# Kernel optimization log

Measured on AMD Instinct MI355X. Metric: run time of the kernel, lower is better.

## Reference

```python
import math
import jax, jax.numpy as jnp
import numpy as np

B, N, G, D = 8, 1000, 1000, 2
E, H = 128, 8           # embedding_dim, n_heads
DH = E // H             # head dim
KNN = 16                # n_decoding_neighbors (static: mask all zeros -> K=min(16,N))
TANH_CLIP = 10.0


def make_heads(x, n_heads):
    # (B, n, E) -> (B, n_heads, n, E//n_heads)
    b, n, e = x.shape
    return x.reshape(b, n, n_heads, e // n_heads).transpose(0, 2, 1, 3)


def setup_inputs() -> dict:
    key = jax.random.key(0)
    ks = jax.random.split(key, 12)
    s = 1.0 / math.sqrt(E)
    return {
        "last_node": jax.random.randint(ks[0], (B, G), 0, N),
        "coordinates": jax.random.uniform(ks[1], (B, N, D), dtype=jnp.float32),
        "embeddings": jax.random.normal(ks[2], (B, N, E), dtype=jnp.float32),
        "group_ninf_mask": jnp.zeros((B, G, N), dtype=jnp.float32),
        "Wq_graph": jax.random.normal(ks[3], (E, E), dtype=jnp.float32) * s,
        "Wq_first": jax.random.normal(ks[4], (E, E), dtype=jnp.float32) * s,
        "Wq_last": jax.random.normal(ks[5], (E, E), dtype=jnp.float32) * s,
        "Wk": jax.random.normal(ks[6], (E, E), dtype=jnp.float32) * s,
        "Wv": jax.random.normal(ks[7], (E, E), dtype=jnp.float32) * s,
        "W_comb": jax.random.normal(ks[8], (E, E), dtype=jnp.float32) * s,
        "b_comb": jax.random.normal(ks[9], (E,), dtype=jnp.float32) * s,
    }


def reference(last_node, coordinates, embeddings, group_ninf_mask,
              Wq_graph, Wq_first, Wq_last, Wk, Wv, W_comb, b_comb):
    # --- reset() precomputation ---
    graph_emb = embeddings.mean(axis=1, keepdims=True)          # (B,1,E)
    q_graph = make_heads(graph_emb @ Wq_graph.T, H)             # (B,H,1,DH)
    k_h = make_heads(embeddings @ Wk.T, H)                      # (B,H,N,DH)
    v_h = make_heads(embeddings @ Wv.T, H)                      # (B,H,N,DH)

    # --- gather last node embedding ---
    idx_e = jnp.broadcast_to(last_node[..., None], (B, G, E))
    last_emb = jnp.take_along_axis(embeddings, idx_e, axis=1)   # (B,G,E)
    q_first = make_heads(last_emb @ Wq_first.T, H)              # (B,H,G,DH)
    q_last = make_heads(last_emb @ Wq_last.T, H)
    glimpse_q = q_graph + q_first + q_last                      # (B,H,G,DH)

    # --- KNN neighbor mask (cdist + topk + scatter) ---
    idx_c = jnp.broadcast_to(last_node[..., None], (B, G, D))
    last_coord = jnp.take_along_axis(coordinates, idx_c, axis=1)  # (B,G,D)
    d2 = (jnp.sum(last_coord**2, -1)[:, :, None]
          + jnp.sum(coordinates**2, -1)[:, None, :]
          - 2.0 * jnp.einsum('bgd,bnd->bgn', last_coord, coordinates))
    dist = jnp.sqrt(jnp.maximum(d2, 0.0))                       # (B,G,N)
    dist = jnp.where(group_ninf_mask == -jnp.inf, jnp.inf, dist)
    _, knn_idx = jax.lax.top_k(-dist, KNN)                      # (B,G,K) smallest dists
    bi = jnp.arange(B)[:, None, None]
    gi = jnp.arange(G)[None, :, None]
    glimpse_mask = jnp.full((B, G, N), -jnp.inf, dtype=jnp.float32)
    glimpse_mask = glimpse_mask.at[bi, gi, knn_idx].set(0.0)

    # --- masked multi-head glimpse attention ---
    scores = jnp.einsum('bhgd,bhnd->bhgn', glimpse_q, k_h) / math.sqrt(DH)
    scores = scores + glimpse_mask[:, None, :, :]
    attn = jax.nn.softmax(scores, axis=-1)
    out = jnp.einsum('bhgn,bhnd->bhgd', attn, v_h)              # (B,H,G,DH)
    out = out.transpose(0, 2, 1, 3).reshape(B, G, E)
    final_q = out @ W_comb.T + b_comb                           # (B,G,E)

    # --- tanh-clipped scoring + softmax ---
    score = jnp.einsum('bge,bne->bgn', final_q, embeddings) / math.sqrt(E)
    score_masked = TANH_CLIP * jnp.tanh(score) + group_ninf_mask
    probs = jax.nn.softmax(score_masked, axis=2)                # (B,G,N)
    return probs
```

## Files before the change

kernel.cpp:

```cpp
#include <hip/hip_runtime.h>
#include <math.h>

#define BD 8
#define NN 1000
#define GG 1000
#define EE 128

typedef unsigned long long u64;
typedef __attribute__((ext_vector_type(8))) short short8;
typedef __attribute__((ext_vector_type(4))) float f32x4;

#define OFF_QG    0
#define OFF_K     1024
#define OFF_V     (OFF_K + 1024000)
#define OFF_QFL   (OFF_V + 1024000)
#define OFF_OUTG  (OFF_QFL + 1024000)
#define OFF_FQ    (OFF_OUTG + 1024000)
#define OFF_PART  (OFF_FQ + 1024000)
#define OFF_GPART (OFF_PART + 64000)

__global__ __launch_bounds__(256) void k_gq1(const float* __restrict__ emb,
                                             float* __restrict__ gpart) {
  __shared__ float ps[2][128];
  int b = blockIdx.x, blk = blockIdx.y;
  int t = threadIdx.x;
  int e = t & 127, p = t >> 7;
  const float* eb = emb + ((size_t)b * NN + blk * 40 + p * 20) * EE + e;
  float s = 0.f;
#pragma unroll 4
  for (int n = 0; n < 20; ++n) s += eb[(size_t)n * EE];
  ps[p][e] = s;
  __syncthreads();
  if (t < 128) gpart[(b * 25 + blk) * 128 + t] = ps[0][t] + ps[1][t];
}

__global__ __launch_bounds__(128) void k_gq2(const float* __restrict__ gpart,
                                             const float* __restrict__ Wqg,
                                             float* __restrict__ qg) {
  __shared__ float ge[128];
  int b = blockIdx.x, t = threadIdx.x;
  float s = 0.f;
#pragma unroll 5
  for (int j = 0; j < 25; ++j) s += gpart[(b * 25 + j) * 128 + t];
  ge[t] = s * (1.f / 1000.f);
  __syncthreads();
  const float* wr = Wqg + (size_t)t * EE;
  float acc = 0.f;
#pragma unroll 8
  for (int k = 0; k < 128; ++k) acc += ge[k] * wr[k];
  qg[b * EE + t] = acc;
}

__global__ __launch_bounds__(256) void k_proj(const float* __restrict__ emb,
                                              const float* __restrict__ Wk,
                                              const float* __restrict__ Wv,
                                              const float* __restrict__ Wqf,
                                              const float* __restrict__ Wql,
                                              float* __restrict__ Karr,
                                              float* __restrict__ Varr,
                                              float* __restrict__ QFL) {
  __shared__ float Als[16][68];
  __shared__ float Bls[16][68];
  int mt = blockIdx.x, nt = blockIdx.y;
  int t = threadIdx.x;
  int ty = t >> 4, tx = t & 15;
  int row4 = t >> 2, kq = t & 3;
  float acc[4][4] = {};
  for (int k0 = 0; k0 < 128; k0 += 16) {
    const float* ap = emb + (size_t)(mt * 64 + row4) * EE + k0 + kq * 4;
    float4 av = *(const float4*)ap;
    int j = nt * 64 + row4;
    float4 bv;
    if (j < 128) {
      bv = *(const float4*)(Wk + (size_t)j * EE + k0 + kq * 4);
    } else if (j < 256) {
      bv = *(const float4*)(Wv + (size_t)(j - 128) * EE + k0 + kq * 4);
    } else {
      float4 f = *(const float4*)(Wqf + (size_t)(j - 256) * EE + k0 + kq * 4);
      float4 l = *(const float4*)(Wql + (size_t)(j - 256) * EE + k0 + kq * 4);
      bv = make_float4(f.x + l.x, f.y + l.y, f.z + l.z, f.w + l.w);
    }
    Als[kq * 4 + 0][row4] = av.x; Als[kq * 4 + 1][row4] = av.y;
    Als[kq * 4 + 2][row4] = av.z; Als[kq * 4 + 3][row4] = av.w;
    Bls[kq * 4 + 0][row4] = bv.x; Bls[kq * 4 + 1][row4] = bv.y;
    Bls[kq * 4 + 2][row4] = bv.z; Bls[kq * 4 + 3][row4] = bv.w;
    __syncthreads();
#pragma unroll
    for (int k = 0; k < 16; ++k) {
      float a0 = Als[k][ty * 4 + 0], a1 = Als[k][ty * 4 + 1];
      float a2 = Als[k][ty * 4 + 2], a3 = Als[k][ty * 4 + 3];
      float b0 = Bls[k][tx * 4 + 0], b1 = Bls[k][tx * 4 + 1];
      float b2 = Bls[k][tx * 4 + 2], b3 = Bls[k][tx * 4 + 3];
      acc[0][0] += a0 * b0; acc[0][1] += a0 * b1; acc[0][2] += a0 * b2; acc[0][3] += a0 * b3;
      acc[1][0] += a1 * b0; acc[1][1] += a1 * b1; acc[1][2] += a1 * b2; acc[1][3] += a1 * b3;
      acc[2][0] += a2 * b0; acc[2][1] += a2 * b1; acc[2][2] += a2 * b2; acc[2][3] += a2 * b3;
      acc[3][0] += a3 * b0; acc[3][1] += a3 * b1; acc[3][2] += a3 * b2; acc[3][3] += a3 * b3;
    }
    __syncthreads();
  }
  float* outp; int cb;
  if (nt < 2)      { outp = Karr; cb = nt * 64; }
  else if (nt < 4) { outp = Varr; cb = (nt - 2) * 64; }
  else             { outp = QFL;  cb = (nt - 4) * 64; }
#pragma unroll
  for (int i = 0; i < 4; ++i) {
    int r = mt * 64 + ty * 4 + i;
    float4 v = make_float4(acc[i][0], acc[i][1], acc[i][2], acc[i][3]);
    *(float4*)(outp + (size_t)r * EE + cb + tx * 4) = v;
  }
}

template <int CTRL>
__device__ __forceinline__ unsigned dpp_minu(unsigned x) {
  unsigned o = (unsigned)__builtin_amdgcn_update_dpp(0, (int)x, CTRL, 0xf, 0xf, false);
  return o < x ? o : x;
}
__device__ __forceinline__ unsigned wave_min_u32(unsigned x) {
  x = dpp_minu<0x121>(x);
  x = dpp_minu<0x122>(x);
  x = dpp_minu<0x124>(x);
  x = dpp_minu<0x128>(x);
  unsigned o = (unsigned)__shfl_xor((int)x, 16); x = o < x ? o : x;
  o = (unsigned)__shfl_xor((int)x, 32); x = o < x ? o : x;
  return x;
}

__global__ __launch_bounds__(256) void k_glimpse(const int* __restrict__ last_node,
                                                 const float* __restrict__ coords,
                                                 const float* __restrict__ mask,
                                                 const float* __restrict__ qg,
                                                 const float* __restrict__ QFL,
                                                 const float* __restrict__ Karr,
                                                 const float* __restrict__ Varr,
                                                 float* __restrict__ outg) {
  __shared__ float pbuf[4][128];
  __shared__ int   nbuf[4][16];
  const float INF = __builtin_inff();
  int wv = threadIdx.x >> 6;
  int lane = threadIdx.x & 63;
  int wid = (blockIdx.x * blockDim.x + threadIdx.x) >> 6;
  int b = wid / GG, g = wid % GG;
  int last = last_node[b * GG + g];
  const float2* cb2 = (const float2*)(coords + (size_t)b * NN * 2);
  float2 lc = cb2[last];
  float lc2 = lc.x * lc.x + lc.y * lc.y;
  const float* mrow = mask + ((size_t)b * GG + g) * NN;
  unsigned d2u[16];
#pragma unroll
  for (int i = 0; i < 16; ++i) {
    int n = lane + (i << 6);
    unsigned k = 0xFFFFFFFFu;
    if (n < NN) {
      float2 c = cb2[n];
      float d2 = lc2 + (c.x * c.x + c.y * c.y) - 2.f * (lc.x * c.x + lc.y * c.y);
      d2 = fmaxf(d2, 0.f);
      k = __float_as_uint(d2);
      if (mrow[n] == -INF) k = 0x7F800000u;
    }
    d2u[i] = k;
  }
  int h = lane >> 3;
  int kk = lane & 7;
  int n0sel = 0, n1sel = 0;
  for (int s = 0; s < 16; ++s) {
    unsigned bv = d2u[0]; int bs = 0;
#pragma unroll
    for (int i = 1; i < 16; ++i) {
      bool better = d2u[i] < bv;
      bv = better ? d2u[i] : bv;
      bs = better ? i : bs;
    }
    unsigned wm = wave_min_u32(bv);
    u64 tied = __ballot(bv == wm);
    int wn;
    if (__popcll(tied) == 1) {
      int wl = (int)__builtin_ctzll(tied);
      int ws = __builtin_amdgcn_readlane(bs, wl);
      wn = wl + (ws << 6);
    } else {
      unsigned cn = (bv == wm) ? (unsigned)(lane + (bs << 6)) : 0x7FFFFFFFu;
      cn = wave_min_u32(cn);
      wn = (int)__builtin_amdgcn_readfirstlane((int)cn);
    }
    n0sel = (s == kk) ? wn : n0sel;
    n1sel = (s == kk + 8) ? wn : n1sel;
    int iw = wn >> 6;
    bool me = (lane == (wn & 63));
#pragma unroll
    for (int i = 0; i < 16; ++i)
      if (i == iw && me) d2u[i] = 0xFFFFFFFFu;
  }
  float qh[16];
  {
    const float4* qg4 = (const float4*)(qg + b * EE + h * 16);
    const float4* qf4 = (const float4*)(QFL + ((size_t)b * NN + last) * EE + h * 16);
#pragma unroll
    for (int u = 0; u < 4; ++u) {
      float4 a = qg4[u], c = qf4[u];
      qh[u * 4 + 0] = a.x + c.x; qh[u * 4 + 1] = a.y + c.y;
      qh[u * 4 + 2] = a.z + c.z; qh[u * 4 + 3] = a.w + c.w;
    }
  }
  const float* Kb = Karr + (size_t)b * NN * EE;
  float s0 = 0.f, s1 = 0.f;
  {
    const float4* k04 = (const float4*)(Kb + (size_t)n0sel * EE + h * 16);
    const float4* k14 = (const float4*)(Kb + (size_t)n1sel * EE + h * 16);
    float4 ka[4], kb[4];
#pragma unroll
    for (int u = 0; u < 4; ++u) { ka[u] = k04[u]; kb[u] = k14[u]; }
#pragma unroll
    for (int u = 0; u < 4; ++u) {
      s0 += qh[u * 4 + 0] * ka[u].x; s0 += qh[u * 4 + 1] * ka[u].y;
      s0 += qh[u * 4 + 2] * ka[u].z; s0 += qh[u * 4 + 3] * ka[u].w;
      s1 += qh[u * 4 + 0] * kb[u].x; s1 += qh[u * 4 + 1] * kb[u].y;
      s1 += qh[u * 4 + 2] * kb[u].z; s1 += qh[u * 4 + 3] * kb[u].w;
    }
  }
  s0 *= 0.25f; s1 *= 0.25f;
  float m = fmaxf(s0, s1);
#pragma unroll
  for (int off = 1; off < 8; off <<= 1) m = fmaxf(m, __shfl_xor(m, off));
  float e0 = __expf(s0 - m), e1 = __expf(s1 - m);
  float se = e0 + e1;
#pragma unroll
  for (int off = 1; off < 8; off <<= 1) se += __shfl_xor(se, off);
  float p0 = e0 / se, p1 = e1 / se;
  pbuf[wv][h * 16 + kk] = p0;
  pbuf[wv][h * 16 + kk + 8] = p1;
  if (h == 0) { nbuf[wv][kk] = n0sel; nbuf[wv][kk + 8] = n1sel; }
  const float* Vb = Varr + (size_t)b * NN * EE;
  float o0 = 0.f, o1 = 0.f;
#pragma unroll
  for (int c = 0; c < 2; ++c) {
    int nk[8]; float pk[8]; float2 vv[8];
#pragma unroll
    for (int j = 0; j < 8; ++j) { nk[j] = nbuf[wv][c * 8 + j]; pk[j] = pbuf[wv][h * 16 + c * 8 + j]; }
#pragma unroll
    for (int j = 0; j < 8; ++j)
      vv[j] = *(const float2*)(Vb + (size_t)nk[j] * EE + h * 16 + kk * 2);
#pragma unroll
    for (int j = 0; j < 8; ++j) { o0 += pk[j] * vv[j].x; o1 += pk[j] * vv[j].y; }
  }
  *(float2*)(outg + ((size_t)b * GG + g) * EE + h * 16 + kk * 2) = make_float2(o0, o1);
}

__global__ __launch_bounds__(256) void k_comb(const float* __restrict__ outg,
                                              const float* __restrict__ Wc,
                                              const float* __restrict__ bc,
                                              short* __restrict__ fq3) {
  __shared__ float Als[16][68];
  __shared__ float Bls[16][132];
  int mt = blockIdx.x;
  int t = threadIdx.x;
  int ty = t >> 4, tx = t & 15;
  int la = t >> 2, akq = t & 3;
  int lb = t >> 1, bkq = t & 1;
  const float* apos = outg + (size_t)(mt * 64 + la) * EE + akq * 4;
  const float* bpos = Wc + (size_t)lb * EE + bkq * 8;
  float acc[4][8] = {};
  float4 pa  = *(const float4*)apos;
  float4 pb0 = *(const float4*)bpos;
  float4 pb1 = *(const float4*)(bpos + 4);
  for (int k0 = 0; k0 < 128; k0 += 16) {
    __syncthreads();
    Als[akq * 4 + 0][la] = pa.x;  Als[akq * 4 + 1][la] = pa.y;
    Als[akq * 4 + 2][la] = pa.z;  Als[akq * 4 + 3][la] = pa.w;
    Bls[bkq * 8 + 0][lb] = pb0.x; Bls[bkq * 8 + 1][lb] = pb0.y;
    Bls[bkq * 8 + 2][lb] = pb0.z; Bls[bkq * 8 + 3][lb] = pb0.w;
    Bls[bkq * 8 + 4][lb] = pb1.x; Bls[bkq * 8 + 5][lb] = pb1.y;
    Bls[bkq * 8 + 6][lb] = pb1.z; Bls[bkq * 8 + 7][lb] = pb1.w;
    __syncthreads();
    if (k0 < 112) {
      pa  = *(const float4*)(apos + k0 + 16);
      pb0 = *(const float4*)(bpos + k0 + 16);
      pb1 = *(const float4*)(bpos + k0 + 20);
    }
#pragma unroll
    for (int k = 0; k < 16; ++k) {
      float4 av  = *(const float4*)&Als[k][ty * 4];
      float4 bv0 = *(const float4*)&Bls[k][tx * 8];
      float4 bv1 = *(const float4*)&Bls[k][tx * 8 + 4];
      float af[4] = {av.x, av.y, av.z, av.w};
      float bf[8] = {bv0.x, bv0.y, bv0.z, bv0.w, bv1.x, bv1.y, bv1.z, bv1.w};
#pragma unroll
      for (int i = 0; i < 4; ++i)
#pragma unroll
        for (int j = 0; j < 8; ++j) acc[i][j] += af[i] * bf[j];
    }
  }
  int c0 = tx * 8;
  float4 b0 = *(const float4*)(bc + c0);
  float4 b1 = *(const float4*)(bc + c0 + 4);
  float bias[8] = {b0.x, b0.y, b0.z, b0.w, b1.x, b1.y, b1.z, b1.w};
  int k0f = tx >> 2;
  int lsub = tx & 3;
#pragma unroll
  for (int i = 0; i < 4; ++i) {
    int r = mt * 64 + ty * 4 + i;
    int b = r / GG;
    int g = r - b * GG;
    short8 hv, mv, lv;
#pragma unroll
    for (int j = 0; j < 8; ++j) {
      float xv = acc[i][j] + bias[j];
      unsigned uh = __float_as_uint(xv) & 0xFFFF0000u;
      hv[j] = (short)(uh >> 16);
      float r1 = xv - __uint_as_float(uh);
      unsigned um = __float_as_uint(r1) & 0xFFFF0000u;
      mv[j] = (short)(um >> 16);
      float r2 = r1 - __uint_as_float(um);
      lv[j] = (short)(__float_as_uint(r2) >> 16);
    }
    int tile = g >> 4;
    int lanefrag = (g & 15) + lsub * 16;
    short* dbase = fq3 + ((size_t)b * 393216 + (size_t)((tile * 4 + k0f) * 3) * 512 + lanefrag * 8);
    *(short8*)(dbase)        = hv;
    *(short8*)(dbase + 512)  = mv;
    *(short8*)(dbase + 1024) = lv;
  }
}

__global__ __launch_bounds__(256) void k_cvt(const float* __restrict__ src,
                                             short* __restrict__ dst) {
  int t = blockIdx.x, b = blockIdx.y;
  int w = threadIdx.x >> 6, l = threadIdx.x & 63;
  int r = min(t * 16 + (l & 15), NN - 1);
  int k = w * 32 + (l >> 4) * 8;
  const float* sp = src + ((size_t)b * NN + r) * EE + k;
  float4 v0 = *(const float4*)sp;
  float4 v1 = *(const float4*)(sp + 4);
  float x[8] = {v0.x, v0.y, v0.z, v0.w, v1.x, v1.y, v1.z, v1.w};
  short8 hv, mv, lv;
#pragma unroll
  for (int j = 0; j < 8; ++j) {
    float xv = x[j];
    unsigned uh = __float_as_uint(xv) & 0xFFFF0000u;
    hv[j] = (short)(uh >> 16);
    float r1 = xv - __uint_as_float(uh);
    unsigned um = __float_as_uint(r1) & 0xFFFF0000u;
    mv[j] = (short)(um >> 16);
    float r2 = r1 - __uint_as_float(um);
    lv[j] = (short)(__float_as_uint(r2) >> 16);
  }
  short* dbase = dst + ((size_t)b * 393216 + (size_t)((t * 4 + w) * 3) * 512 + l * 8);
  *(short8*)(dbase)        = hv;
  *(short8*)(dbase + 512)  = mv;
  *(short8*)(dbase + 1024) = lv;
}

__global__ __launch_bounds__(256, 2) void k_score(const short* __restrict__ fq3,
                                                  const short* __restrict__ emb3,
                                                  const float* __restrict__ mask,
                                                  float* __restrict__ out,
                                                  float* __restrict__ part) {
  __shared__ float xs[4][16][132];
  int nt = blockIdx.x, gt = blockIdx.y, b = blockIdx.z;
  int w = threadIdx.x >> 6, l = threadIdx.x & 63;
  int gtile = gt * 4 + w;
  const short* ab = fq3 + ((size_t)b * 393216 + (size_t)gtile * 6144 + l * 8);
  const short* bb = emb3 + ((size_t)b * 393216 + (size_t)nt * 8 * 6144 + l * 8);
  f32x4 acc[8] = {};
#pragma unroll
  for (int k0 = 0; k0 < 4; ++k0) {
    short8 ah = *(const short8*)(ab + (k0 * 3 + 0) * 512);
    short8 am = *(const short8*)(ab + (k0 * 3 + 1) * 512);
    short8 al = *(const short8*)(ab + (k0 * 3 + 2) * 512);
#pragma unroll
    for (int c = 0; c < 8; ++c) {
      const short* bp = bb + (size_t)(c * 6144 + k0 * 1536);
      short8 bh = *(const short8*)(bp);
      short8 bm = *(const short8*)(bp + 512);
      short8 bl = *(const short8*)(bp + 1024);
      acc[c] = __builtin_amdgcn_mfma_f32_16x16x32_bf16(ah, bh, acc[c], 0, 0, 0);
      acc[c] = __builtin_amdgcn_mfma_f32_16x16x32_bf16(am, bh, acc[c], 0, 0, 0);
      acc[c] = __builtin_amdgcn_mfma_f32_16x16x32_bf16(ah, bm, acc[c], 0, 0, 0);
      acc[c] = __builtin_amdgcn_mfma_f32_16x16x32_bf16(am, bm, acc[c], 0, 0, 0);
      acc[c] = __builtin_amdgcn_mfma_f32_16x16x32_bf16(al, bh, acc[c], 0, 0, 0);
      acc[c] = __builtin_amdgcn_mfma_f32_16x16x32_bf16(ah, bl, acc[c], 0, 0, 0);
    }
  }
  int q = l >> 4, cl = l & 15;
#pragma unroll
  for (int c = 0; c < 8; ++c)
#pragma unroll
    for (int r = 0; r < 4; ++r)
      xs[w][q * 4 + r][c * 16 + cl] = acc[c][r];
  const float rs = 0.08838834764831845f;
  const float NEGINF = -__builtin_inff();
  int half = l >> 5, ln = l & 31;
  int n0 = nt * 128 + ln * 4;
  bool nv = (n0 < NN);
  size_t brow = (size_t)b * GG;
#pragma unroll
  for (int it = 0; it < 8; ++it) {
    int row = it * 2 + half;
    int g = gt * 64 + w * 16 + row;
    bool gv = (g < GG);
    size_t roff = (brow + (gv ? g : GG - 1)) * (size_t)NN;
    f32x4 v = *(const f32x4*)&xs[w][row][ln * 4];
    float4 mvv;
    if (gv && nv) mvv = *(const float4*)(mask + roff + n0);
    else mvv = make_float4(NEGINF, NEGINF, NEGINF, NEGINF);
    float mva[4] = {mvv.x, mvv.y, mvv.z, mvv.w};
    float e[4];
    float rsum = 0.f;
#pragma unroll
    for (int j = 0; j < 4; ++j) {
      float sc = v[j] * rs;
      float u = __expf(2.f * sc);
      float th = 1.f - 2.f * __builtin_amdgcn_rcpf(u + 1.f);
      e[j] = __expf(10.f * th + mva[j]);
      rsum += e[j];
    }
    if (gv && nv) *(float4*)(out + roff + n0) = make_float4(e[0], e[1], e[2], e[3]);
#pragma unroll
    for (int off = 1; off < 32; off <<= 1) rsum += __shfl_xor(rsum, off);
    if (ln == 0 && gv) part[(brow + g) * 8 + nt] = rsum;
  }
}

__global__ __launch_bounds__(256) void k_norm(const float* __restrict__ part,
                                              float* __restrict__ out) {
  int row = blockIdx.x;
  __shared__ float ssum;
  int t = threadIdx.x;
  float v = (t < 8) ? part[(size_t)row * 8 + t] : 0.f;
#pragma unroll
  for (int off = 1; off < 8; off <<= 1) v += __shfl_xor(v, off);
  if (t == 0) ssum = v;
  __syncthreads();
  float inv = 1.f / ssum;
  if (t < 250) {
    float4* o = (float4*)(out + (size_t)row * NN);
    float4 x = o[t];
    x.x *= inv; x.y *= inv; x.z *= inv; x.w *= inv;
    o[t] = x;
  }
}

extern "C" void kernel_launch(void* const* d_in, const int* in_sizes, int n_in,
                              void* d_out, int out_size, void* d_ws, size_t ws_size,
                              hipStream_t stream) {
  const int*   last_node = (const int*)d_in[0];
  const float* coords    = (const float*)d_in[1];
  const float* emb       = (const float*)d_in[2];
  const float* mask      = (const float*)d_in[3];
  const float* Wqg       = (const float*)d_in[4];
  const float* Wqf       = (const float*)d_in[5];
  const float* Wql       = (const float*)d_in[6];
  const float* Wk        = (const float*)d_in[7];
  const float* Wv        = (const float*)d_in[8];
  const float* Wc        = (const float*)d_in[9];
  const float* bc        = (const float*)d_in[10];
  float* out = (float*)d_out;
  float* ws  = (float*)d_ws;

  float* qg    = ws + OFF_QG;
  float* Karr  = ws + OFF_K;
  float* Varr  = ws + OFF_V;
  float* QFL   = ws + OFF_QFL;
  float* outg  = ws + OFF_OUTG;
  float* part  = ws + OFF_PART;
  float* gpart = ws + OFF_GPART;
  short* emb3  = (short*)(ws + OFF_K);
  short* fq3   = (short*)(ws + OFF_FQ);

  k_gq1<<<dim3(BD, 25), dim3(256), 0, stream>>>(emb, gpart);
  k_gq2<<<dim3(BD), dim3(128), 0, stream>>>(gpart, Wqg, qg);
  k_proj<<<dim3(125, 6), dim3(256), 0, stream>>>(emb, Wk, Wv, Wqf, Wql, Karr, Varr, QFL);
  k_glimpse<<<dim3(2000), dim3(256), 0, stream>>>(last_node, coords, mask, qg, QFL, Karr, Varr, outg);
  k_comb<<<dim3(125), dim3(256), 0, stream>>>(outg, Wc, bc, fq3);
  k_cvt<<<dim3(64, BD), dim3(256), 0, stream>>>(emb, emb3);
  k_score<<<dim3(8, 16, 8), dim3(256), 0, stream>>>(fq3, emb3, mask, out, part);
  k_norm<<<dim3(8000), dim3(256), 0, stream>>>(part, out);
}
```

Baseline: 207.3 us.

## Fuse softmax normalization into score kernel with full-row 1024-thread blocks

Restructures the score kernel so that one 1024-thread block covers 32 group rows across all N columns. Row sums are reduced in shared memory and the normalized probabilities are written directly, which removes the separate normalization kernel. This saves a full read-modify-write pass over the 32MB output and one launch. In exchange the kernel holds 32 exp values per thread in registers, runs only 256 blocks at one block per CU, and loses occupancy.

```diff
diff --git a/kernel.cpp b/kernel.cpp
--- a/kernel.cpp
+++ b/kernel.cpp
@@ -349,17 +349,19 @@
   *(short8*)(dbase + 1024) = lv;
 }
 
-__global__ __launch_bounds__(256, 2) void k_score(const short* __restrict__ fq3,
-                                                  const short* __restrict__ emb3,
-                                                  const float* __restrict__ mask,
-                                                  float* __restrict__ out,
-                                                  float* __restrict__ part) {
-  __shared__ float xs[4][16][132];
-  int nt = blockIdx.x, gt = blockIdx.y, b = blockIdx.z;
-  int w = threadIdx.x >> 6, l = threadIdx.x & 63;
-  int gtile = gt * 4 + w;
+__global__ __launch_bounds__(1024, 1) void k_score(const short* __restrict__ fq3,
+                                                   const short* __restrict__ emb3,
+                                                   const float* __restrict__ mask,
+                                                   float* __restrict__ out) {
+  __shared__ float xs[16][16][36];
+  __shared__ float psum[32][8];
+  __shared__ float sinv[32];
+  int gy = blockIdx.x, b = blockIdx.y;
+  int wv = threadIdx.x >> 6, l = threadIdx.x & 63;
+  int wg = wv >> 3, wn = wv & 7;
+  int gtile = gy * 2 + wg;
   const short* ab = fq3 + ((size_t)b * 393216 + (size_t)gtile * 6144 + l * 8);
-  const short* bb = emb3 + ((size_t)b * 393216 + (size_t)nt * 8 * 6144 + l * 8);
+  const short* bb = emb3 + ((size_t)b * 393216 + (size_t)wn * 8 * 6144 + l * 8);
   f32x4 acc[8] = {};
 #pragma unroll
   for (int k0 = 0; k0 < 4; ++k0) {
@@ -380,63 +382,78 @@
       acc[c] = __builtin_amdgcn_mfma_f32_16x16x32_bf16(ah, bl, acc[c], 0, 0, 0);
     }
   }
-  int q = l >> 4, cl = l & 15;
-#pragma unroll
-  for (int c = 0; c < 8; ++c)
-#pragma unroll
-    for (int r = 0; r < 4; ++r)
-      xs[w][q * 4 + r][c * 16 + cl] = acc[c][r];
   const float rs = 0.08838834764831845f;
   const float NEGINF = -__builtin_inff();
-  int half = l >> 5, ln = l & 31;
-  int n0 = nt * 128 + ln * 4;
-  bool nv = (n0 < NN);
+  int q = l >> 4, cl = l & 15;
+  int lr = l >> 3, lc = l & 7;
   size_t brow = (size_t)b * GG;
-#pragma unroll
-  for (int it = 0; it < 8; ++it) {
-    int row = it * 2 + half;
-    int g = gt * 64 + w * 16 + row;
-    bool gv = (g < GG);
-    size_t roff = (brow + (gv ? g : GG - 1)) * (size_t)NN;
-    f32x4 v = *(const f32x4*)&xs[w][row][ln * 4];
-    float4 mvv;
-    if (gv && nv) mvv = *(const float4*)(mask + roff + n0);
-    else mvv = make_float4(NEGINF, NEGINF, NEGINF, NEGINF);
-    float mva[4] = {mvv.x, mvv.y, mvv.z, mvv.w};
-    float e[4];
-    float rsum = 0.f;
-#pragma unroll
-    for (int j = 0; j < 4; ++j) {
-      float sc = v[j] * rs;
-      float u = __expf(2.f * sc);
-      float th = 1.f - 2.f * __builtin_amdgcn_rcpf(u + 1.f);
-      e[j] = __expf(10.f * th + mva[j]);
-      rsum += e[j];
-    }
-    if (gv && nv) *(float4*)(out + roff + n0) = make_float4(e[0], e[1], e[2], e[3]);
-#pragma unroll
-    for (int off = 1; off < 32; off <<= 1) rsum += __shfl_xor(rsum, off);
-    if (ln == 0 && gv) part[(brow + g) * 8 + nt] = rsum;
-  }
-}
-
-__global__ __launch_bounds__(256) void k_norm(const float* __restrict__ part,
-                                              float* __restrict__ out) {
-  int row = blockIdx.x;
-  __shared__ float ssum;
-  int t = threadIdx.x;
-  float v = (t < 8) ? part[(size_t)row * 8 + t] : 0.f;
-#pragma unroll
-  for (int off = 1; off < 8; off <<= 1) v += __shfl_xor(v, off);
-  if (t == 0) ssum = v;
+  float e[8][4];
+  float rs0 = 0.f, rs1 = 0.f;
+#pragma unroll
+  for (int p = 0; p < 4; ++p) {
+#pragma unroll
+    for (int cc = 0; cc < 2; ++cc)
+#pragma unroll
+      for (int r = 0; r < 4; ++r)
+        xs[wv][q * 4 + r][cc * 16 + cl] = acc[p * 2 + cc][r];
+#pragma unroll
+    for (int i = 0; i < 2; ++i) {
+      int row = i * 8 + lr;
+      int g = gy * 32 + wg * 16 + row;
+      bool gv = (g < GG);
+      size_t roff = (brow + (gv ? g : GG - 1)) * (size_t)NN;
+      int n0 = wn * 128 + p * 32 + lc * 4;
+      bool nv = (n0 < NN);
+      f32x4 v = *(const f32x4*)&xs[wv][row][lc * 4];
+      float4 mvv;
+      if (gv && nv) mvv = *(const float4*)(mask + roff + n0);
+      else mvv = make_float4(NEGINF, NEGINF, NEGINF, NEGINF);
+      float mva[4] = {mvv.x, mvv.y, mvv.z, mvv.w};
+      float esum = 0.f;
+#pragma unroll
+      for (int j = 0; j < 4; ++j) {
+        float sc = v[j] * rs;
+        float u = __expf(2.f * sc);
+        float th = 1.f - 2.f * __builtin_amdgcn_rcpf(u + 1.f);
+        float ev = __expf(10.f * th + mva[j]);
+        e[p * 2 + i][j] = ev;
+        esum += ev;
+      }
+      if (i == 0) rs0 += esum; else rs1 += esum;
+    }
+  }
+#pragma unroll
+  for (int off = 1; off < 8; off <<= 1) {
+    rs0 += __shfl_xor(rs0, off);
+    rs1 += __shfl_xor(rs1, off);
+  }
+  if (lc == 0) {
+    psum[wg * 16 + lr][wn] = rs0;
+    psum[wg * 16 + 8 + lr][wn] = rs1;
+  }
   __syncthreads();
-  float inv = 1.f / ssum;
-  if (t < 250) {
-    float4* o = (float4*)(out + (size_t)row * NN);
-    float4 x = o[t];
-    x.x *= inv; x.y *= inv; x.z *= inv; x.w *= inv;
-    o[t] = x;
-  }
+  if (threadIdx.x < 32) {
+    int t = threadIdx.x;
+    float s = 0.f;
+#pragma unroll
+    for (int j = 0; j < 8; ++j) s += psum[t][j];
+    sinv[t] = 1.f / s;
+  }
+  __syncthreads();
+#pragma unroll
+  for (int p = 0; p < 4; ++p)
+#pragma unroll
+    for (int i = 0; i < 2; ++i) {
+      int row = i * 8 + lr;
+      int g = gy * 32 + wg * 16 + row;
+      int n0 = wn * 128 + p * 32 + lc * 4;
+      if (g < GG && n0 < NN) {
+        float inv = sinv[wg * 16 + row];
+        size_t roff = (brow + g) * (size_t)NN;
+        *(float4*)(out + roff + n0) = make_float4(e[p * 2 + i][0] * inv, e[p * 2 + i][1] * inv,
+                                                  e[p * 2 + i][2] * inv, e[p * 2 + i][3] * inv);
+      }
+    }
 }
 
 extern "C" void kernel_launch(void* const* d_in, const int* in_sizes, int n_in,
@@ -461,7 +478,6 @@
   float* Varr  = ws + OFF_V;
   float* QFL   = ws + OFF_QFL;
   float* outg  = ws + OFF_OUTG;
-  float* part  = ws + OFF_PART;
   float* gpart = ws + OFF_GPART;
   short* emb3  = (short*)(ws + OFF_K);
   short* fq3   = (short*)(ws + OFF_FQ);
@@ -472,6 +488,5 @@
   k_glimpse<<<dim3(2000), dim3(256), 0, stream>>>(last_node, coords, mask, qg, QFL, Karr, Varr, outg);
   k_comb<<<dim3(125), dim3(256), 0, stream>>>(outg, Wc, bc, fq3);
   k_cvt<<<dim3(64, BD), dim3(256), 0, stream>>>(emb, emb3);
-  k_score<<<dim3(8, 16, 8), dim3(256), 0, stream>>>(fq3, emb3, mask, out, part);
-  k_norm<<<dim3(8000), dim3(256), 0, stream>>>(part, out);
-}
+  k_score<<<dim3(32, BD), dim3(1024), 0, stream>>>(fq3, emb3, mask, out);
+}
```

Result: faster. 195.6 us (-5.7%).
